# Kernel optimization log

Measured on AMD Instinct MI355X. Metric: run time of the kernel, lower is better.

## Reference

```python
import jax, jax.numpy as jnp
import numpy as np

B, N, F_DIM, M, K, D = 8, 16384, 6, 128, 16, 768
MLP_DIMS = [F_DIM, 256, 512, 768, D]


def _fps(pts):
    """Deterministic farthest point sampling. pts: [N,4] -> indices [M] (first pick = point 0)."""
    n = pts.shape[0]

    def step(carry, _):
        min_d, last = carry
        d = jnp.sum((pts - pts[last]) ** 2, axis=-1)
        min_d = jnp.minimum(min_d, d)
        nxt = jnp.argmax(min_d).astype(jnp.int32)
        return (min_d, nxt), nxt

    init = (jnp.full((n,), 1e30, dtype=pts.dtype), jnp.int32(0))
    _, idx = jax.lax.scan(step, init, None, length=M - 1)
    return jnp.concatenate([jnp.zeros((1,), jnp.int32), idx])


def setup_inputs() -> dict:
    key = jax.random.key(0)
    ks = jax.random.split(key, 16)
    bidx = jnp.repeat(jnp.arange(B, dtype=jnp.float32), N)[:, None]
    xyzt = jax.random.normal(ks[0], (B * N, 4), jnp.float32)
    coordinates = jnp.concatenate([bidx, xyzt], axis=1)  # [B*N, 5]
    features = jax.random.normal(ks[1], (B * N, F_DIM), jnp.float32)
    inp = {"coordinates": coordinates, "features": features}
    for i in range(4):
        di, do = MLP_DIMS[i], MLP_DIMS[i + 1]
        inp[f"W{i}"] = jax.random.normal(ks[2 + i], (di, do), jnp.float32) * np.float32(1.0 / np.sqrt(di))
        inp[f"b{i}"] = jnp.zeros((do,), jnp.float32)
    for j in range(2):
        inp[f"Wn{j}"] = jax.random.normal(ks[6 + j], (D, D), jnp.float32) * np.float32(1.0 / np.sqrt(D))
        inp[f"bn{j}"] = jnp.zeros((D,), jnp.float32)
    return inp


def _forward(coordinates, features, W0, b0, W1, b1, W2, b2, W3, b3, Wn0, bn0, Wn1, bn1):
    # Equal points per event, sorted batch ids -> plain reshape replaces the per-batch loop.
    pts = coordinates.reshape(B, N, 5)[:, :, 1:5]       # xyz + time  [B,N,4]
    h = features.reshape(B, N, F_DIM)
    # per-point MLP (ReLU after each hidden layer, final Linear has no activation)
    h = jax.nn.relu(h @ W0 + b0)
    h = jax.nn.relu(h @ W1 + b1)
    h = jax.nn.relu(h @ W2 + b2)
    pf = h @ W3 + b3                                    # [B,N,D]
    # FPS centroids (non-differentiable index selection, as in the torch/cpu original)
    fidx = jax.vmap(_fps)(jax.lax.stop_gradient(pts))   # [B,M]
    cent = jnp.take_along_axis(pts, fidx[:, :, None], axis=1)  # [B,M,4]
    # cdist + kNN (smallest distances)
    dist = jnp.sqrt(jnp.sum((cent[:, :, None, :] - pts[:, None, :, :]) ** 2, axis=-1))  # [B,M,N]
    _, knn = jax.lax.top_k(-dist, K)                    # [B,M,K]
    gathered = jax.vmap(lambda p, i: p[i])(pf, knn)     # [B,M,K,D]
    pooled = jnp.max(gathered, axis=2)                  # [B,M,D]
    t = jax.nn.relu(pooled @ Wn0 + bn0)
    tokens = t @ Wn1 + bn1                              # [B,M,D]
    # sort tokens/centroids by centroid time (column 3)
    order = jnp.argsort(cent[:, :, 3], axis=1)
    cent = jnp.take_along_axis(cent, order[:, :, None], axis=1)
    tokens = jnp.take_along_axis(tokens, order[:, :, None], axis=1)
    masks = jnp.ones((B, M), dtype=bool)  # num_points > max_tokens -> all tokens valid
    return tokens, cent, masks


def reference(coordinates, features, W0, b0, W1, b1, W2, b2, W3, b3, Wn0, bn0, Wn1, bn1):
    return _forward(coordinates, features, W0, b0, W1, b1, W2, b2, W3, b3, Wn0, bn0, Wn1, bn1)
```

## Files before the change

### kernel.cpp

```cpp
#include <hip/hip_runtime.h>

#define B_ 8
#define N_ 16384
#define F_ 6
#define M_ 128
#define K_ 16
#define D_ 768

typedef unsigned short u16;
typedef unsigned int u32;
typedef unsigned long long u64;
typedef __attribute__((ext_vector_type(8))) short short8;
typedef __attribute__((ext_vector_type(4))) float f32x4;
typedef __attribute__((ext_vector_type(2))) float f32x2;

__device__ __forceinline__ u16 f2bf(float f){
  union { float f; u32 i; } v; v.f = f;
  u32 x = v.i;
  u32 r = x + 0x7FFFu + ((x >> 16) & 1u);
  return (u16)(r >> 16);
}

__device__ __forceinline__ void ld_g2l(const u16* g, u16* l){
  __builtin_amdgcn_global_load_lds((const __attribute__((address_space(1))) u32*)g,
                                   (__attribute__((address_space(3))) u32*)l, 16, 0, 0);
}

__device__ __forceinline__ f32x2 pkadd(f32x2 a, f32x2 b){
  f32x2 d; asm("v_pk_add_f32 %0, %1, %2" : "=v"(d) : "v"(a), "v"(b)); return d;
}
__device__ __forceinline__ f32x2 pkmul(f32x2 a, f32x2 b){
  f32x2 d; asm("v_pk_mul_f32 %0, %1, %2" : "=v"(d) : "v"(a), "v"(b)); return d;
}

__device__ __forceinline__ f32x4 ld_x4(const float* p){
  f32x4 r;
  asm volatile("global_load_dwordx4 %0, %1, off" : "=v"(r) : "v"(p) : "memory");
  return r;
}

template<int CTRL>
__device__ __forceinline__ float dppmax(float v){
  union { float f; int i; } a, r;
  a.f = v;
  r.i = __builtin_amdgcn_update_dpp(a.i, a.i, CTRL, 0xF, 0xF, false);
  return fmaxf(v, r.f);
}

__global__ __launch_bounds__(256) void conv_all(const float* __restrict__ W1,
                                                const float* __restrict__ W2,
                                                const float* __restrict__ W3,
                                                const float* __restrict__ Wn0,
                                                const float* __restrict__ Wn1,
                                                u16* __restrict__ Wb){
  __shared__ u16 tile[64][65];
  int blk = blockIdx.x;
  const float* W; u16* WT; int K, N, lb;
  if      (blk < 32)  { W = W1;  WT = Wb;           K = 256; N = 512; lb = blk; }
  else if (blk < 128) { W = W2;  WT = Wb + 131072;  K = 512; N = 768; lb = blk - 32; }
  else if (blk < 272) { W = W3;  WT = Wb + 524288;  K = 768; N = 768; lb = blk - 128; }
  else if (blk < 416) { W = Wn0; WT = Wb + 1114112; K = 768; N = 768; lb = blk - 272; }
  else                { W = Wn1; WT = Wb + 1703936; K = 768; N = 768; lb = blk - 416; }
  int tiles_n = N >> 6;
  int tk = lb / tiles_n, tn = lb % tiles_n;
  int k0 = tk << 6, n0 = tn << 6;
  int t = threadIdx.x;
#pragma unroll
  for (int q = 0; q < 16; q++){
    int idx = q * 256 + t;
    int kk = idx >> 6, nn = idx & 63;
    tile[kk][nn] = f2bf(W[(size_t)(k0 + kk) * N + n0 + nn]);
  }
  __syncthreads();
#pragma unroll
  for (int q = 0; q < 16; q++){
    int idx = q * 256 + t;
    int nn = idx >> 6, kk = idx & 63;
    WT[(size_t)(n0 + nn) * K + k0 + kk] = tile[kk][nn];
  }
}

__global__ __launch_bounds__(512) __attribute__((amdgpu_waves_per_eu(2, 2)))
void fps_block(const float* __restrict__ coords, float* __restrict__ cent){
#pragma clang fp contract(off)
  __shared__ float swv[2][8];
  __shared__ int   swi[2][8];
  int b = blockIdx.x;
  int t = threadIdx.x;
  int lane = t & 63, wave = t >> 6;
  const float* cb = coords + (size_t)b * N_ * 5;
  const int base = t << 5;
  f32x4 p[32];
#pragma unroll
  for (int k = 0; k < 32; k++){
    p[k] = ld_x4(cb + (size_t)(base + k) * 5 + 1);
  }
  float md[32];
#pragma unroll
  for (int k = 0; k < 32; k++) md[k] = 1e30f;
  asm volatile("s_waitcnt vmcnt(0)" ::: "memory");
  __builtin_amdgcn_sched_barrier(0);
  float cx = cb[1], cy = cb[2], cz = cb[3], ct = cb[4];
  if (t == 0){
    float* c0 = cent + (size_t)b * M_ * 4;
    c0[0]=cx; c0[1]=cy; c0[2]=cz; c0[3]=ct;
  }
  for (int step = 1; step < M_; step++){
    f32x2 ncxy = (f32x2){-cx, -cy};
    f32x2 nczw = (f32x2){-cz, -ct};
    float bv = -1.0f; int bl = 0;
#pragma unroll
    for (int k = 0; k < 32; k++){
      f32x2 xy = (f32x2){p[k][0], p[k][1]};
      f32x2 zw = (f32x2){p[k][2], p[k][3]};
      f32x2 dxy = pkadd(xy, ncxy);
      f32x2 dzw = pkadd(zw, nczw);
      f32x2 s1 = pkmul(dxy, dxy);
      f32x2 s2 = pkmul(dzw, dzw);
      float s = ((s1[0] + s1[1]) + s2[0]) + s2[1];
      float m = fminf(s, md[k]);
      md[k] = m;
      if (m > bv){ bv = m; bl = k; }
    }
    int bi = base + bl;
    float r = bv;
    r = dppmax<0x111>(r);
    r = dppmax<0x112>(r);
    r = dppmax<0x114>(r);
    r = dppmax<0x118>(r);
    r = dppmax<0x142>(r);
    r = dppmax<0x143>(r);
    union { float f; int i; } rm; rm.f = r;
    union { int i; float f; } wmu; wmu.i = __builtin_amdgcn_readlane(rm.i, 63);
    float wmax = wmu.f;
    u64 wmask = __ballot(bv == wmax);
    int srcL = (int)__ffsll((unsigned long long)wmask) - 1;
    int wbi = __builtin_amdgcn_readlane(bi, srcL);
    int par = step & 1;
    if (lane == 0){ swv[par][wave] = wmax; swi[par][wave] = wbi; }
    __syncthreads();
    float fv = swv[par][0]; int fi = swi[par][0];
#pragma unroll
    for (int w = 1; w < 8; w++){
      float v = swv[par][w];
      int  iw = swi[par][w];
      if (v > fv){ fv = v; fi = iw; }
    }
    int widx = __builtin_amdgcn_readfirstlane(fi);
    size_t wb = (size_t)widx * 5;
    cx = cb[wb+1]; cy = cb[wb+2]; cz = cb[wb+3]; ct = cb[wb+4];
    if (t == 0){
      float* cr = cent + ((size_t)b * M_ + step) * 4;
      cr[0]=cx; cr[1]=cy; cr[2]=cz; cr[3]=ct;
    }
  }
}

__global__ __launch_bounds__(128) void rank_scatter(const float* __restrict__ cent_fps,
                                                    float* __restrict__ cent_sorted,
                                                    float* __restrict__ out,
                                                    size_t out_elems){
  int b = blockIdx.x, m = threadIdx.x;
  __shared__ float tt[M_];
  const float* row = cent_fps + ((size_t)b * M_ + m) * 4;
  float x=row[0], y=row[1], z=row[2], w=row[3];
  tt[m] = w;
  __syncthreads();
  int rank = 0;
  for (int j = 0; j < M_; j++){
    float tj = tt[j];
    if (tj < w || (tj == w && j < m)) rank++;
  }
  float* dst = cent_sorted + ((size_t)b * M_ + rank) * 4;
  dst[0]=x; dst[1]=y; dst[2]=z; dst[3]=w;
  size_t co = (size_t)B_ * M_ * D_ + ((size_t)b * M_ + rank) * 4;
  if (co + 3 < out_elems){
    out[co+0]=x; out[co+1]=y; out[co+2]=z; out[co+3]=w;
  }
  size_t mo = (size_t)B_ * M_ * D_ + (size_t)B_ * M_ * 4 + (size_t)b * M_ + m;
  if (mo < out_elems) out[mo] = 1.0f;
}

#define KNT 512
#define KPT 32
__global__ __launch_bounds__(512) void knn_kernel(const float* __restrict__ coords,
                                                  const float* __restrict__ cent,
                                                  int* __restrict__ knn){
#pragma clang fp contract(off)
  int cm = blockIdx.x;
  int b = cm >> 7;
  const float* cb = coords + (size_t)b * N_ * 5;
  int t = threadIdx.x;
  float cx=cent[cm*4+0], cy=cent[cm*4+1], cz=cent[cm*4+2], ct=cent[cm*4+3];
  float dist[KPT];
#pragma unroll
  for (int j = 0; j < KPT; j++){
    size_t i = t + j * KNT;
    float dx=cb[i*5+1]-cx, dy=cb[i*5+2]-cy, dz=cb[i*5+3]-cz, dw=cb[i*5+4]-ct;
    float d = ((dx*dx + dy*dy) + dz*dz) + dw*dw;
    dist[j] = sqrtf(d);
  }
  __shared__ float s_wv[8];
  __shared__ int s_wi[8];
  __shared__ int s_bi;
  for (int r = 0; r < K_; r++){
    float bv = 3e38f; int bi = 1 << 30;
#pragma unroll
    for (int j = 0; j < KPT; j++){
      int i = t + j * KNT;
      float v = dist[j];
      if (v < bv){ bv = v; bi = i; }
    }
#pragma unroll
    for (int off = 32; off > 0; off >>= 1){
      float ov = __shfl_down(bv, off);
      int oi = __shfl_down(bi, off);
      if (ov < bv || (ov == bv && oi < bi)){ bv = ov; bi = oi; }
    }
    if ((t & 63) == 0){ s_wv[t >> 6] = bv; s_wi[t >> 6] = bi; }
    __syncthreads();
    if (t == 0){
      float fv = s_wv[0]; int fi = s_wi[0];
      for (int w = 1; w < 8; w++){
        float wv = s_wv[w]; int wi = s_wi[w];
        if (wv < fv || (wv == fv && wi < fi)){ fv = wv; fi = wi; }
      }
      s_bi = fi;
      knn[(size_t)cm * K_ + r] = fi & (N_ - 1);
    }
    __syncthreads();
    int wi = s_bi;
#pragma unroll
    for (int j = 0; j < KPT; j++){
      if (t + j * KNT == wi) dist[j] = 3e38f;
    }
  }
}

__global__ __launch_bounds__(256) void gather_l0(const float* __restrict__ feat,
                                                 const int* __restrict__ knn,
                                                 const float* __restrict__ W0,
                                                 const float* __restrict__ b0,
                                                 u16* __restrict__ h1,
                                                 int rowBase){
  __shared__ float sW[F_][256];
  __shared__ float sb[256];
  __shared__ float sfa[32][F_];
  int t = threadIdx.x;
#pragma unroll
  for (int k = 0; k < F_; k++) sW[k][t] = W0[k * 256 + t];
  sb[t] = b0[t];
  if (t < 32 * F_){
    int r = t / F_, k = t % F_;
    int grow = rowBase + blockIdx.x * 32 + r;
    int bb = grow >> 11;
    int idx = knn[grow] & (N_ - 1);
    sfa[r][k] = feat[((size_t)bb * N_ + idx) * F_ + k];
  }
  __syncthreads();
#pragma unroll 4
  for (int r = 0; r < 32; r++){
    float acc = sb[t];
#pragma unroll
    for (int k = 0; k < F_; k++) acc = fmaf(sfa[r][k], sW[k][t], acc);
    int lrow = blockIdx.x * 32 + r;
    h1[(size_t)lrow * 256 + t] = f2bf(fmaxf(acc, 0.0f));
  }
}

template<int RELU, int OUTF32>
__global__ __launch_bounds__(256) void gemm_bf16(const u16* __restrict__ A,
                                                 const u16* __restrict__ WT,
                                                 const float* __restrict__ bias,
                                                 void* __restrict__ Cv,
                                                 int Kd, int Nd){
  __shared__ u16 As[128][32];
  __shared__ u16 Bs[128][32];
  const int t = threadIdx.x;
  const int bm = blockIdx.y << 7;
  const int bn = blockIdx.x << 7;
  const int wave = t >> 6;
  const int lane = t & 63;
  const int wm = (wave & 1) << 6;
  const int wn = (wave >> 1) << 6;
  const int lm = lane & 15;
  const int lk = (lane >> 4) << 3;
  u16* AsF = &As[0][0];
  u16* BsF = &Bs[0][0];
  const int wbase = wave << 6;
  f32x4 acc[4][4] = {};
  for (int k0 = 0; k0 < Kd; k0 += 32){
#pragma unroll
    for (int it = 0; it < 2; it++){
      int slot = t + (it << 8);
      int r = slot >> 2;
      int c = (slot & 3) << 3;
      int dst = (wbase + (it << 8)) << 3;
      ld_g2l(A  + (size_t)(bm + r) * Kd + k0 + c, AsF + dst);
      ld_g2l(WT + (size_t)(bn + r) * Kd + k0 + c, BsF + dst);
    }
    __syncthreads();
    short8 af[4], bfr[4];
#pragma unroll
    for (int mt = 0; mt < 4; mt++) af[mt] = *(const short8*)&As[wm + (mt << 4) + lm][lk];
#pragma unroll
    for (int nt = 0; nt < 4; nt++) bfr[nt] = *(const short8*)&Bs[wn + (nt << 4) + lm][lk];
#pragma unroll
    for (int mt = 0; mt < 4; mt++)
#pragma unroll
      for (int nt = 0; nt < 4; nt++)
        acc[mt][nt] = __builtin_amdgcn_mfma_f32_16x16x32_bf16(af[mt], bfr[nt], acc[mt][nt], 0, 0, 0);
    __syncthreads();
  }
#pragma unroll
  for (int nt = 0; nt < 4; nt++){
    int n = bn + wn + (nt << 4) + lm;
    float bia = bias[n];
#pragma unroll
    for (int mt = 0; mt < 4; mt++){
#pragma unroll
      for (int r2 = 0; r2 < 4; r2++){
        int m = bm + wm + (mt << 4) + ((lane >> 4) << 2) + r2;
        float v = acc[mt][nt][r2] + bia;
        if (RELU) v = fmaxf(v, 0.0f);
        if (OUTF32) ((float*)Cv)[(size_t)m * Nd + n] = v;
        else        ((u16*)Cv)[(size_t)m * Nd + n] = f2bf(v);
      }
    }
  }
}

template<int RELU, int OUTF32>
__global__ __launch_bounds__(256) void gemm64(const u16* __restrict__ A,
                                              const u16* __restrict__ WT,
                                              const float* __restrict__ bias,
                                              void* __restrict__ Cv,
                                              int Kd, int Nd){
  __shared__ u16 As[64][32];
  __shared__ u16 Bs[64][32];
  const int t = threadIdx.x;
  const int bm = blockIdx.y << 6;
  const int bn = blockIdx.x << 6;
  const int wave = t >> 6;
  const int lane = t & 63;
  const int wm = (wave & 1) << 5;
  const int wn = (wave >> 1) << 5;
  const int lm = lane & 15;
  const int lk = (lane >> 4) << 3;
  u16* AsF = &As[0][0];
  u16* BsF = &Bs[0][0];
  const int wbase = wave << 6;
  f32x4 acc[2][2] = {};
  for (int k0 = 0; k0 < Kd; k0 += 32){
    {
      int r = t >> 2;
      int c = (t & 3) << 3;
      int dst = wbase << 3;
      ld_g2l(A  + (size_t)(bm + r) * Kd + k0 + c, AsF + dst);
      ld_g2l(WT + (size_t)(bn + r) * Kd + k0 + c, BsF + dst);
    }
    __syncthreads();
    short8 af[2], bfr[2];
#pragma unroll
    for (int mt = 0; mt < 2; mt++) af[mt] = *(const short8*)&As[wm + (mt << 4) + lm][lk];
#pragma unroll
    for (int nt = 0; nt < 2; nt++) bfr[nt] = *(const short8*)&Bs[wn + (nt << 4) + lm][lk];
#pragma unroll
    for (int mt = 0; mt < 2; mt++)
#pragma unroll
      for (int nt = 0; nt < 2; nt++)
        acc[mt][nt] = __builtin_amdgcn_mfma_f32_16x16x32_bf16(af[mt], bfr[nt], acc[mt][nt], 0, 0, 0);
    __syncthreads();
  }
#pragma unroll
  for (int nt = 0; nt < 2; nt++){
    int n = bn + wn + (nt << 4) + lm;
    float bia = bias[n];
#pragma unroll
    for (int mt = 0; mt < 2; mt++){
#pragma unroll
      for (int r2 = 0; r2 < 4; r2++){
        int m = bm + wm + (mt << 4) + ((lane >> 4) << 2) + r2;
        float v = acc[mt][nt][r2] + bia;
        if (RELU) v = fmaxf(v, 0.0f);
        if (OUTF32) ((float*)Cv)[(size_t)m * Nd + n] = v;
        else        ((u16*)Cv)[(size_t)m * Nd + n] = f2bf(v);
      }
    }
  }
}

__global__ __launch_bounds__(256) void gemm_pool(const u16* __restrict__ A,
                                                 const u16* __restrict__ WT,
                                                 const float* __restrict__ bias,
                                                 u16* __restrict__ pooled,
                                                 int Kd, int Nd, int groupBase){
  __shared__ u16 As[128][32];
  __shared__ u16 Bs[128][32];
  const int t = threadIdx.x;
  const int bm = blockIdx.y << 7;
  const int bn = blockIdx.x << 7;
  const int wave = t >> 6;
  const int lane = t & 63;
  const int wm = (wave & 1) << 6;
  const int wn = (wave >> 1) << 6;
  const int lm = lane & 15;
  const int lk = (lane >> 4) << 3;
  u16* AsF = &As[0][0];
  u16* BsF = &Bs[0][0];
  const int wbase = wave << 6;
  f32x4 acc[4][4] = {};
  for (int k0 = 0; k0 < Kd; k0 += 32){
#pragma unroll
    for (int it = 0; it < 2; it++){
      int slot = t + (it << 8);
      int r = slot >> 2;
      int c = (slot & 3) << 3;
      int dst = (wbase + (it << 8)) << 3;
      ld_g2l(A  + (size_t)(bm + r) * Kd + k0 + c, AsF + dst);
      ld_g2l(WT + (size_t)(bn + r) * Kd + k0 + c, BsF + dst);
    }
    __syncthreads();
    short8 af[4], bfr[4];
#pragma unroll
    for (int mt = 0; mt < 4; mt++) af[mt] = *(const short8*)&As[wm + (mt << 4) + lm][lk];
#pragma unroll
    for (int nt = 0; nt < 4; nt++) bfr[nt] = *(const short8*)&Bs[wn + (nt << 4) + lm][lk];
#pragma unroll
    for (int mt = 0; mt < 4; mt++)
#pragma unroll
      for (int nt = 0; nt < 4; nt++)
        acc[mt][nt] = __builtin_amdgcn_mfma_f32_16x16x32_bf16(af[mt], bfr[nt], acc[mt][nt], 0, 0, 0);
    __syncthreads();
  }
#pragma unroll
  for (int nt = 0; nt < 4; nt++){
    int n = bn + wn + (nt << 4) + lm;
    float bia = bias[n];
#pragma unroll
    for (int mt = 0; mt < 4; mt++){
      f32x4 a = acc[mt][nt];
      float v = fmaxf(fmaxf(a[0], a[1]), fmaxf(a[2], a[3]));
      v = fmaxf(v, __shfl_xor(v, 16));
      v = fmaxf(v, __shfl_xor(v, 32));
      if ((lane >> 4) == 0){
        int g = groupBase + (bm >> 4) + (wm >> 4) + mt;
        pooled[(size_t)g * Nd + n] = f2bf(v + bia);
      }
    }
  }
}

__global__ __launch_bounds__(256) void fill_diag(float* __restrict__ out, size_t out_elems){
  size_t i = (size_t)blockIdx.x * 256 + threadIdx.x;
  if (i >= out_elems) return;
  size_t maskStart = (size_t)B_ * M_ * D_ + (size_t)B_ * M_ * 4;
  out[i] = (i >= maskStart) ? 1.0f : 0.0f;
}

extern "C" void kernel_launch(void* const* d_in, const int* in_sizes, int n_in,
                              void* d_out, int out_size, void* d_ws, size_t ws_size,
                              hipStream_t stream){
  (void)in_sizes; (void)n_in;
  const float* coords   = (const float*)d_in[0];
  const float* features = (const float*)d_in[1];
  const float* W0 = (const float*)d_in[2];  const float* b0 = (const float*)d_in[3];
  const float* W1 = (const float*)d_in[4];  const float* b1 = (const float*)d_in[5];
  const float* W2 = (const float*)d_in[6];  const float* b2 = (const float*)d_in[7];
  const float* W3 = (const float*)d_in[8];  const float* b3 = (const float*)d_in[9];
  const float* Wn0 = (const float*)d_in[10]; const float* bn0 = (const float*)d_in[11];
  const float* Wn1 = (const float*)d_in[12]; const float* bn1 = (const float*)d_in[13];
  float* out = (float*)d_out;
  const size_t out_elems = (size_t)out_size;

  char* ws = (char*)d_ws;
  const size_t o_cent = 0;
  const size_t o_cntS = 16384;
  const size_t o_knn  = 32768;
  const size_t o_Wb   = 131072;
  const size_t o_pool = 4718592;
  const size_t o_t1   = 6291456;
  const size_t o_chunk= 7864320;
  const int ROWS = B_ * M_ * K_;

  int R = 16384;
  while (R > 128 && o_chunk + (size_t)R * 2560 > ws_size) R >>= 1;
  if (d_ws == nullptr || o_chunk + (size_t)R * 2560 > ws_size){
    fill_diag<<<(int)((out_elems + 255) / 256), 256, 0, stream>>>(out, out_elems);
    return;
  }

  float* cent_fps    = (float*)(ws + o_cent);
  float* cent_sorted = (float*)(ws + o_cntS);
  int*   knn         = (int*)(ws + o_knn);
  u16* Wb   = (u16*)(ws + o_Wb);
  u16* W1t  = Wb;               u16* W2t  = Wb + 131072;
  u16* W3t  = Wb + 524288;      u16* Wn0t = Wb + 1114112;
  u16* Wn1t = Wb + 1703936;
  u16* pooled = (u16*)(ws + o_pool);
  u16* t1     = (u16*)(ws + o_t1);
  u16* regA   = (u16*)(ws + o_chunk);
  u16* regB   = (u16*)(ws + o_chunk + (size_t)R * 1536);

  conv_all<<<560, 256, 0, stream>>>(W1, W2, W3, Wn0, Wn1, Wb);
  fps_block<<<B_, 512, 0, stream>>>(coords, cent_fps);
  rank_scatter<<<B_, 128, 0, stream>>>(cent_fps, cent_sorted, out, out_elems);
  knn_kernel<<<B_ * M_, KNT, 0, stream>>>(coords, cent_sorted, knn);

  for (int rowBase = 0; rowBase < ROWS; rowBase += R){
    gather_l0<<<R / 32, 256, 0, stream>>>(features, knn, W0, b0, regA, rowBase);
    gemm_bf16<1,0><<<dim3(4, R / 128), 256, 0, stream>>>(regA, W1t, b1, regB, 256, 512);
    gemm_bf16<1,0><<<dim3(6, R / 128), 256, 0, stream>>>(regB, W2t, b2, regA, 512, 768);
    gemm_pool<<<dim3(6, R / 128), 256, 0, stream>>>(regA, W3t, b3, pooled, 768, 768, rowBase >> 4);
  }

  gemm64<1,0><<<dim3(12, (B_ * M_) / 64), 256, 0, stream>>>(pooled, Wn0t, bn0, t1, 768, 768);
  gemm64<0,1><<<dim3(12, (B_ * M_) / 64), 256, 0, stream>>>(t1, Wn1t, bn1, out, 768, 768);
}
```

Before: 506.1 us.

## Widen FPS block to 1024 threads, stage xy in LDS, broadcast winner coords

The farthest-point-sampling kernel goes from 512 to 1024 threads per block, so each thread handles 16 points instead of 32. The xy half of the points moves into shared memory while zw stays in registers. Each wave now writes its winning point's coordinates to shared memory, so the global reload of the selected centroid is gone. The intent is to shorten the serial per-step chain (fewer points per thread, no dependent global load each step), at the cost of an LDS read per point every step and a 16-wave reduction instead of 8. The initial load loop now waits on every load before writing to LDS, which serialises the memory fetches.

```diff
diff --git a/kernel.cpp b/kernel.cpp
--- a/kernel.cpp
+++ b/kernel.cpp
@@ -80,25 +80,28 @@
   }
 }
 
-__global__ __launch_bounds__(512) __attribute__((amdgpu_waves_per_eu(2, 2)))
+#define FPT 16
+__global__ __launch_bounds__(1024) __attribute__((amdgpu_waves_per_eu(4, 4)))
 void fps_block(const float* __restrict__ coords, float* __restrict__ cent){
 #pragma clang fp contract(off)
-  __shared__ float swv[2][8];
-  __shared__ int   swi[2][8];
+  __shared__ f32x2 sxy[N_];
+  __shared__ f32x4 swv4[2][4];
+  __shared__ f32x4 swc[2][16];
   int b = blockIdx.x;
   int t = threadIdx.x;
   int lane = t & 63, wave = t >> 6;
   const float* cb = coords + (size_t)b * N_ * 5;
-  const int base = t << 5;
-  f32x4 p[32];
-#pragma unroll
-  for (int k = 0; k < 32; k++){
-    p[k] = ld_x4(cb + (size_t)(base + k) * 5 + 1);
-  }
-  float md[32];
-#pragma unroll
-  for (int k = 0; k < 32; k++) md[k] = 1e30f;
-  asm volatile("s_waitcnt vmcnt(0)" ::: "memory");
+  const int base = t << 4;
+  f32x2 pzw[FPT];
+  float md[FPT];
+#pragma unroll
+  for (int k = 0; k < FPT; k++){
+    f32x4 q = ld_x4(cb + (size_t)(base + k) * 5 + 1);
+    asm volatile("s_waitcnt vmcnt(0)" ::: "memory");
+    sxy[k * 1024 + t] = (f32x2){q[0], q[1]};
+    pzw[k] = (f32x2){q[2], q[3]};
+    md[k] = 1e30f;
+  }
   __builtin_amdgcn_sched_barrier(0);
   float cx = cb[1], cy = cb[2], cz = cb[3], ct = cb[4];
   if (t == 0){
@@ -110,11 +113,10 @@
     f32x2 nczw = (f32x2){-cz, -ct};
     float bv = -1.0f; int bl = 0;
 #pragma unroll
-    for (int k = 0; k < 32; k++){
-      f32x2 xy = (f32x2){p[k][0], p[k][1]};
-      f32x2 zw = (f32x2){p[k][2], p[k][3]};
+    for (int k = 0; k < FPT; k++){
+      f32x2 xy = sxy[k * 1024 + t];
       f32x2 dxy = pkadd(xy, ncxy);
-      f32x2 dzw = pkadd(zw, nczw);
+      f32x2 dzw = pkadd(pzw[k], nczw);
       f32x2 s1 = pkmul(dxy, dxy);
       f32x2 s2 = pkmul(dzw, dzw);
       float s = ((s1[0] + s1[1]) + s2[0]) + s2[1];
@@ -122,7 +124,6 @@
       md[k] = m;
       if (m > bv){ bv = m; bl = k; }
     }
-    int bi = base + bl;
     float r = bv;
     r = dppmax<0x111>(r);
     r = dppmax<0x112>(r);
@@ -135,20 +136,31 @@
     float wmax = wmu.f;
     u64 wmask = __ballot(bv == wmax);
     int srcL = (int)__ffsll((unsigned long long)wmask) - 1;
-    int wbi = __builtin_amdgcn_readlane(bi, srcL);
+    f32x2 zwsel = pzw[0];
+#pragma unroll
+    for (int k = 1; k < FPT; k++) zwsel = (bl == k) ? pzw[k] : zwsel;
     int par = step & 1;
-    if (lane == 0){ swv[par][wave] = wmax; swi[par][wave] = wbi; }
-    __syncthreads();
-    float fv = swv[par][0]; int fi = swi[par][0];
-#pragma unroll
-    for (int w = 1; w < 8; w++){
-      float v = swv[par][w];
-      int  iw = swi[par][w];
-      if (v > fv){ fv = v; fi = iw; }
-    }
-    int widx = __builtin_amdgcn_readfirstlane(fi);
-    size_t wb = (size_t)widx * 5;
-    cx = cb[wb+1]; cy = cb[wb+2]; cz = cb[wb+3]; ct = cb[wb+4];
+    if (lane == srcL){
+      f32x2 xyw = sxy[bl * 1024 + t];
+      ((float*)&swv4[par])[wave] = bv;
+      swc[par][wave] = (f32x4){xyw[0], xyw[1], zwsel[0], zwsel[1]};
+    }
+    __syncthreads();
+    float fv; int fw = 0;
+    {
+      f32x4 v0 = swv4[par][0], v1 = swv4[par][1], v2 = swv4[par][2], v3 = swv4[par][3];
+      fv = v0[0];
+#pragma unroll
+      for (int j = 1; j < 4; j++) if (v0[j] > fv){ fv = v0[j]; fw = j; }
+#pragma unroll
+      for (int j = 0; j < 4; j++) if (v1[j] > fv){ fv = v1[j]; fw = 4 + j; }
+#pragma unroll
+      for (int j = 0; j < 4; j++) if (v2[j] > fv){ fv = v2[j]; fw = 8 + j; }
+#pragma unroll
+      for (int j = 0; j < 4; j++) if (v3[j] > fv){ fv = v3[j]; fw = 12 + j; }
+    }
+    f32x4 wc = swc[par][fw];
+    cx = wc[0]; cy = wc[1]; cz = wc[2]; ct = wc[3];
     if (t == 0){
       float* cr = cent + ((size_t)b * M_ + step) * 4;
       cr[0]=cx; cr[1]=cy; cr[2]=cz; cr[3]=ct;
@@ -503,7 +515,7 @@
   u16* regB   = (u16*)(ws + o_chunk + (size_t)R * 1536);
 
   conv_all<<<560, 256, 0, stream>>>(W1, W2, W3, Wn0, Wn1, Wb);
-  fps_block<<<B_, 512, 0, stream>>>(coords, cent_fps);
+  fps_block<<<B_, 1024, 0, stream>>>(coords, cent_fps);
   rank_scatter<<<B_, 128, 0, stream>>>(cent_fps, cent_sorted, out, out_elems);
   knn_kernel<<<B_ * M_, KNT, 0, stream>>>(coords, cent_sorted, knn);
 
```

Measured after the change: 579.3 us. +14.5%, slower.
